# Optimization experiments

Hardware: AMD Instinct MI355X
Metric: run time of the kernel (lower is better)

Reference implementation:

```python
import jax, jax.numpy as jnp
import numpy as np

B, S, D_MODEL, N_HEADS, HEAD_DIM = 4, 2048, 1024, 16, 64
NEG = -1e9


def apply_rope_real(x, cos_f, sin_f):
    # x: [B, H, S, D]; cos_f/sin_f: [S, D//2] broadcast over B, H
    x_even = x[..., ::2]
    x_odd = x[..., 1::2]
    out_even = x_even * cos_f - x_odd * sin_f
    out_odd = x_even * sin_f + x_odd * cos_f
    return jnp.stack([out_even, out_odd], axis=-1).reshape(x.shape)


def setup_inputs() -> dict:
    key = jax.random.key(0)
    ks = jax.random.split(key, 8)
    x = jax.random.normal(ks[0], (B, S, D_MODEL), dtype=jnp.float32)
    # RoPE tables: theta_i = 10000^{-2i/d}, angles = pos * theta
    inv_freq = 1.0 / (10000.0 ** (jnp.arange(0, HEAD_DIM, 2, dtype=jnp.float32) / HEAD_DIM))
    angles = jnp.arange(S, dtype=jnp.float32)[:, None] * inv_freq[None, :]  # [S, D/2]
    cos_freqs = jnp.cos(angles)
    sin_freqs = jnp.sin(angles)
    causal_mask = jnp.where(jnp.tril(jnp.ones((S, S), dtype=bool)), 0.0, NEG).astype(jnp.float32)
    scale = 0.02
    w_q = jax.random.normal(ks[1], (D_MODEL, D_MODEL), dtype=jnp.float32) * scale
    w_k = jax.random.normal(ks[2], (D_MODEL, D_MODEL), dtype=jnp.float32) * scale
    w_v = jax.random.normal(ks[3], (D_MODEL, D_MODEL), dtype=jnp.float32) * scale
    w_o = jax.random.normal(ks[4], (D_MODEL, D_MODEL), dtype=jnp.float32) * scale
    return {"x": x, "cos_freqs": cos_freqs, "sin_freqs": sin_freqs,
            "causal_mask": causal_mask, "w_q": w_q, "w_k": w_k, "w_v": w_v, "w_o": w_o}


def reference(x, cos_freqs, sin_freqs, causal_mask, w_q, w_k, w_v, w_o):
    batch, seq_len, _ = x.shape
    scale = 1.0 / jnp.sqrt(jnp.float32(HEAD_DIM))
    # torch Linear: y = x @ W.T
    def proj(w):
        return (x @ w.T).reshape(batch, seq_len, N_HEADS, HEAD_DIM).transpose(0, 2, 1, 3)
    q = apply_rope_real(proj(w_q), cos_freqs, sin_freqs)
    k = apply_rope_real(proj(w_k), cos_freqs, sin_freqs)
    v = proj(w_v)
    attn = jnp.einsum('bhqd,bhkd->bhqk', q, k) * scale + causal_mask
    attn = jax.nn.softmax(attn, axis=-1)
    out = jnp.einsum('bhqk,bhkd->bhqd', attn, v)
    out = out.transpose(0, 2, 1, 3).reshape(batch, seq_len, -1)
    return out @ w_o.T
```

## Files before the change

### kernel.cpp

```cpp
#include <hip/hip_runtime.h>
#include <stdint.h>

#define B_  4
#define S_  2048
#define DM_ 1024
#define NH_ 16
#define HD_ 64

typedef unsigned short ushort_t;
typedef __bf16 bf16x8 __attribute__((ext_vector_type(8)));
typedef float  floatx4 __attribute__((ext_vector_type(4)));
typedef float  floatx16 __attribute__((ext_vector_type(16)));

__device__ __forceinline__ float bf2f(ushort_t u) {
    union { unsigned int i; float f; } v; v.i = ((unsigned int)u) << 16; return v.f;
}
__device__ __forceinline__ ushort_t f2bf(float f) {
    union { float f; unsigned int i; } v; v.f = f;
    unsigned int x = v.i;
    return (ushort_t)((x + 0x7fffu + ((x >> 16) & 1u)) >> 16);
}
__device__ __forceinline__ unsigned int pack_bf16_trunc(float lo, float hi) {
    union { float f; unsigned int u; } a, b;
    a.f = lo; b.f = hi;
    return __builtin_amdgcn_perm(b.u, a.u, 0x07060302u);
}

__global__ __launch_bounds__(256) void cvt_all_kernel(
    const float* __restrict__ x,  const float* __restrict__ wq,
    const float* __restrict__ wk, const float* __restrict__ wv,
    const float* __restrict__ wo,
    ushort_t* __restrict__ xb,  ushort_t* __restrict__ wqb,
    ushort_t* __restrict__ wkb, ushort_t* __restrict__ wvb,
    ushort_t* __restrict__ wob)
{
    const int blk = blockIdx.x;
    const float* src; ushort_t* dst; int off;
    if (blk < 8192)       { src = x;  dst = xb;  off = blk; }
    else if (blk < 9216)  { src = wq; dst = wqb; off = blk - 8192; }
    else if (blk < 10240) { src = wk; dst = wkb; off = blk - 9216; }
    else if (blk < 11264) { src = wv; dst = wvb; off = blk - 10240; }
    else                  { src = wo; dst = wob; off = blk - 11264; }
    const int i = off * 256 + threadIdx.x;
    float4 v = ((const float4*)src)[i];
    ushort4 o; o.x = f2bf(v.x); o.y = f2bf(v.y); o.z = f2bf(v.z); o.w = f2bf(v.w);
    ((ushort4*)dst)[i] = o;
}

__global__ __launch_bounds__(512, 2) void gemm_bt_kernel(
    const ushort_t* __restrict__ A,
    const ushort_t* __restrict__ B0, const ushort_t* __restrict__ B1,
    const ushort_t* __restrict__ B2,
    void* __restrict__ C0, void* __restrict__ C1, void* __restrict__ C2,
    int M, int N, int K, int mode)
{
    __shared__ ushort_t As[2][16384];
    __shared__ ushort_t Bs[2][16384];

    const int z = blockIdx.z;
    const ushort_t* Bw = z == 0 ? B0 : z == 1 ? B1 : B2;
    void* Cv           = z == 0 ? C0 : z == 1 ? C1 : C2;

    const int tid  = threadIdx.x;
    const int wave = tid >> 6, lane = tid & 63;
    const int l15 = lane & 15, quad = lane >> 4;
    const int wr = wave >> 2, wc = wave & 3;
    const int mbase = blockIdx.x * 256;
    const int nbase = blockIdx.y * 256;
    const int NT = K >> 6;

    const int srow = lane >> 3;
    const int schk = (lane & 7) ^ srow;

    auto stageA = [&](int b, int t, int h) {
#pragma unroll
        for (int j = 0; j < 2; ++j) {
            const int idx = wave * 2 + j;
            const int r = h * 128 + idx * 8 + srow;
            const ushort_t* src = A + (size_t)(mbase + r) * K + t * 64 + schk * 8;
            __builtin_amdgcn_global_load_lds(
                (const __attribute__((address_space(1))) unsigned int*)src,
                (__attribute__((address_space(3))) unsigned int*)(&As[b][h * 8192 + idx * 512 + lane * 8]),
                16, 0, 0);
        }
    };
    auto stageB = [&](int b, int t, int h) {
#pragma unroll
        for (int j = 0; j < 2; ++j) {
            const int idx = wave * 2 + j;
            const int r = h * 128 + idx * 8 + srow;
            const ushort_t* src = Bw + (size_t)(nbase + r) * K + t * 64 + schk * 8;
            __builtin_amdgcn_global_load_lds(
                (const __attribute__((address_space(1))) unsigned int*)src,
                (__attribute__((address_space(3))) unsigned int*)(&Bs[b][h * 8192 + idx * 512 + lane * 8]),
                16, 0, 0);
        }
    };

    floatx4 acc[8][4] = {};

    stageA(0, 0, 0); stageA(0, 0, 1);
    stageB(0, 0, 0); stageB(0, 0, 1);
    stageB(1, 1, 0); stageB(1, 1, 1);
    asm volatile("s_waitcnt vmcnt(4)" ::: "memory");
    __builtin_amdgcn_s_barrier();

    auto do_tile = [&](int t, int bt) {
        bf16x8 a0[2][4], a1[2][4], bv0[2][2], bv1[2][2];
#pragma unroll
        for (int kk = 0; kk < 2; ++kk) {
#pragma unroll
            for (int f = 0; f < 4; ++f) {
                const int row = wr * 128 + f * 16 + l15;
                a0[kk][f] = *(const bf16x8*)&As[bt][row * 64 + (((kk << 2) | quad) ^ (l15 & 7)) * 8];
            }
#pragma unroll
            for (int g = 0; g < 2; ++g) {
                const int row = wc * 64 + g * 16 + l15;
                bv0[kk][g] = *(const bf16x8*)&Bs[bt][row * 64 + (((kk << 2) | quad) ^ (l15 & 7)) * 8];
            }
        }
        if (t + 1 < NT) stageA(bt ^ 1, t + 1, 0);
        __builtin_amdgcn_s_barrier();
        asm volatile("s_waitcnt lgkmcnt(0)" ::: "memory");
        __builtin_amdgcn_s_setprio(1);
#pragma unroll
        for (int kk = 0; kk < 2; ++kk)
#pragma unroll
            for (int mt = 0; mt < 4; ++mt)
#pragma unroll
                for (int nt = 0; nt < 2; ++nt)
                    acc[mt][nt] = __builtin_amdgcn_mfma_f32_16x16x32_bf16(
                        a0[kk][mt], bv0[kk][nt], acc[mt][nt], 0, 0, 0);
        __builtin_amdgcn_s_setprio(0);
        __builtin_amdgcn_s_barrier();

#pragma unroll
        for (int kk = 0; kk < 2; ++kk)
#pragma unroll
            for (int g = 0; g < 2; ++g) {
                const int row = wc * 64 + 32 + g * 16 + l15;
                bv1[kk][g] = *(const bf16x8*)&Bs[bt][row * 64 + (((kk << 2) | quad) ^ (l15 & 7)) * 8];
            }
        if (t + 1 < NT) stageA(bt ^ 1, t + 1, 1);
        __builtin_amdgcn_s_barrier();
        asm volatile("s_waitcnt lgkmcnt(0)" ::: "memory");
        __builtin_amdgcn_s_setprio(1);
#pragma unroll
        for (int kk = 0; kk < 2; ++kk)
#pragma unroll
            for (int mt = 0; mt < 4; ++mt)
#pragma unroll
                for (int nt = 0; nt < 2; ++nt)
                    acc[mt][2 + nt] = __builtin_amdgcn_mfma_f32_16x16x32_bf16(
                        a0[kk][mt], bv1[kk][nt], acc[mt][2 + nt], 0, 0, 0);
        __builtin_amdgcn_s_setprio(0);
        __builtin_amdgcn_s_barrier();

#pragma unroll
        for (int kk = 0; kk < 2; ++kk)
#pragma unroll
            for (int f = 0; f < 4; ++f) {
                const int row = wr * 128 + 64 + f * 16 + l15;
                a1[kk][f] = *(const bf16x8*)&As[bt][row * 64 + (((kk << 2) | quad) ^ (l15 & 7)) * 8];
            }
        if (t + 2 < NT) stageB(bt, t + 2, 0);
        __builtin_amdgcn_s_barrier();
        asm volatile("s_waitcnt lgkmcnt(0)" ::: "memory");
        __builtin_amdgcn_s_setprio(1);
#pragma unroll
        for (int kk = 0; kk < 2; ++kk)
#pragma unroll
            for (int mt = 0; mt < 4; ++mt)
#pragma unroll
                for (int nt = 0; nt < 2; ++nt)
                    acc[4 + mt][2 + nt] = __builtin_amdgcn_mfma_f32_16x16x32_bf16(
                        a1[kk][mt], bv1[kk][nt], acc[4 + mt][2 + nt], 0, 0, 0);
        __builtin_amdgcn_s_setprio(0);
        __builtin_amdgcn_s_barrier();

        if (t + 2 < NT) stageB(bt, t + 2, 1);
        __builtin_amdgcn_s_barrier();
        __builtin_amdgcn_s_setprio(1);
#pragma unroll
        for (int kk = 0; kk < 2; ++kk)
#pragma unroll
            for (int mt = 0; mt < 4; ++mt)
#pragma unroll
                for (int nt = 0; nt < 2; ++nt)
                    acc[4 + mt][nt] = __builtin_amdgcn_mfma_f32_16x16x32_bf16(
                        a1[kk][mt], bv0[kk][nt], acc[4 + mt][nt], 0, 0, 0);
        __builtin_amdgcn_s_setprio(0);
        if (t < NT - 2) { asm volatile("s_waitcnt vmcnt(4)" ::: "memory"); }
        else            { asm volatile("s_waitcnt vmcnt(0)" ::: "memory"); }
        __builtin_amdgcn_s_barrier();
    };

    for (int t = 0; t < NT; t += 2) {
        do_tile(t, 0);
        do_tile(t + 1, 1);
    }

    const bool vtmode = (mode == 0) && (z == 2);
#pragma unroll
    for (int mt = 0; mt < 8; ++mt) {
#pragma unroll
        for (int nt = 0; nt < 4; ++nt) {
            const int col = nbase + wc * 64 + nt * 16 + l15;
            const int m0  = mbase + wr * 128 + mt * 16 + quad * 4;
            if (vtmode) {
                const int b = m0 >> 11, s = m0 & 2047;
                const int hh = col >> 6, d = col & 63;
                uint2 pk;
                pk.x = (unsigned)f2bf(acc[mt][nt][0]) | ((unsigned)f2bf(acc[mt][nt][1]) << 16);
                pk.y = (unsigned)f2bf(acc[mt][nt][2]) | ((unsigned)f2bf(acc[mt][nt][3]) << 16);
                *(uint2*)&((ushort_t*)Cv)[((size_t)((b * NH_ + hh) * HD_ + d)) * S_ + s] = pk;
            } else if (mode == 0) {
#pragma unroll
                for (int r = 0; r < 4; ++r) {
                    const int m = m0 + r;
                    const int b = m >> 11, s = m & 2047;
                    const int hh = col >> 6, d = col & 63;
                    ((ushort_t*)Cv)[(((size_t)(b * NH_ + hh)) * S_ + s) * HD_ + d] =
                        f2bf(acc[mt][nt][r]);
                }
            } else {
#pragma unroll
                for (int r = 0; r < 4; ++r)
                    ((float*)Cv)[(size_t)(m0 + r) * N + col] = acc[mt][nt][r];
            }
        }
    }
}

#define QSCALE 0.1803368801f
__global__ __launch_bounds__(256) void rope_kernel(
    ushort_t* __restrict__ q, ushort_t* __restrict__ k,
    const float* __restrict__ cf, const float* __restrict__ sf)
{
    const int idx = blockIdx.x * 256 + threadIdx.x;
    const int j = idx & 31;
    const int s = (idx >> 5) & (S_ - 1);
    const float c  = cf[s * 32 + j];
    const float sn = sf[s * 32 + j];
    const size_t base = (size_t)idx * 2;
    float qe = bf2f(q[base]), qo = bf2f(q[base + 1]);
    q[base]     = f2bf((qe * c - qo * sn) * QSCALE);
    q[base + 1] = f2bf((qe * sn + qo * c) * QSCALE);
    float ke = bf2f(k[base]), ko = bf2f(k[base + 1]);
    k[base]     = f2bf(ke * c - ko * sn);
    k[base + 1] = f2bf(ke * sn + ko * c);
}

__global__ __launch_bounds__(256, 2) void attn_kernel(
    const ushort_t* __restrict__ Qg, const ushort_t* __restrict__ Kg,
    const ushort_t* __restrict__ Vg, ushort_t* __restrict__ Og)
{
    __shared__ ushort_t Ks[64 * 72];
    __shared__ ushort_t Vt[64 * 72];
    __shared__ ushort_t Pt[4][32 * 64];

    const int pair = blockIdx.x;
    const int bh   = blockIdx.y;
    const int tid  = threadIdx.x;
    const int wave = tid >> 6, lane = tid & 63;
    const int l31 = lane & 31, h = lane >> 5;

    const size_t bh_off = (size_t)bh * S_ * HD_;
    const int trow = tid >> 3;
    const int tcol = (tid & 7) * 8;
    const int pswz = (l31 & 7) << 3;
    const int b_out = bh >> 4, h_out = bh & 15;

#pragma unroll 1
    for (int seg = 0; seg < 2; ++seg) {
        const int qtile = seg ? (15 - pair) : pair;
        const int qbase = qtile * 128;
        const int nkt   = 2 * qtile + 2;
        const int qrow  = qbase + wave * 32 + l31;

        bf16x8 qf[4];
#pragma unroll
        for (int ks = 0; ks < 4; ++ks)
            qf[ks] = *(const bf16x8*)(Qg + bh_off + (size_t)qrow * HD_ + ks * 16 + h * 8);

        float m_run = -1e30f, l_run = 0.f;
        floatx16 o_acc[2] = {};

        for (int kt = 0; kt < nkt; ++kt) {
            const int kbase = kt * 64;
            __syncthreads();
#pragma unroll
            for (int r = 0; r < 2; ++r) {
                const int row = trow + r * 32;
                *(bf16x8*)(Ks + row * 72 + tcol) =
                    *(const bf16x8*)(Kg + bh_off + (size_t)(kbase + row) * HD_ + tcol);
                const int c = tid + r * 256;
                const int d = c >> 3, k0 = (c & 7) * 8;
                bf16x8 vv = *(const bf16x8*)(Vg + bh_off + (size_t)d * S_ + kbase + k0);
                *(bf16x8*)(Vt + d * 72 + (k0 ^ (((d >> 3) & 7) << 3))) = vv;
            }
            __syncthreads();

            if (kbase > qbase + wave * 32 + 31) continue;

            floatx16 st[2] = {};
#pragma unroll
            for (int nt = 0; nt < 2; ++nt) {
                const ushort_t* kr = Ks + (nt * 32 + l31) * 72 + h * 8;
#pragma unroll
                for (int ks = 0; ks < 4; ++ks) {
                    bf16x8 kf = *(const bf16x8*)(kr + ks * 16);
                    st[nt] = __builtin_amdgcn_mfma_f32_32x32x16_bf16(kf, qf[ks], st[nt], 0, 0, 0);
                }
            }
            if (kbase + 63 > qbase + wave * 32) {
#pragma unroll
                for (int nt = 0; nt < 2; ++nt) {
                    const int key0 = kbase + nt * 32 + 4 * h;
#pragma unroll
                    for (int c = 0; c < 4; ++c)
#pragma unroll
                        for (int r = 0; r < 4; ++r)
                            if (key0 + 8 * c + r > qrow) st[nt][c * 4 + r] = -1e9f;
                }
            }
            float mx = st[0][0];
#pragma unroll
            for (int nt = 0; nt < 2; ++nt)
#pragma unroll
                for (int i = 0; i < 16; ++i) mx = fmaxf(mx, st[nt][i]);
            mx = fmaxf(mx, __shfl_xor(mx, 32, 64));
            const float mnew = fmaxf(m_run, mx);
            const float alpha = __builtin_amdgcn_exp2f(m_run - mnew);
            m_run = mnew;
            float sum = 0.f;
#pragma unroll
            for (int nt = 0; nt < 2; ++nt)
#pragma unroll
                for (int i = 0; i < 16; ++i) {
                    const float p = __builtin_amdgcn_exp2f(st[nt][i] - mnew);
                    st[nt][i] = p; sum += p;
                }
            sum += __shfl_xor(sum, 32, 64);
            l_run = l_run * alpha + sum;
#pragma unroll
            for (int dt = 0; dt < 2; ++dt)
#pragma unroll
                for (int i = 0; i < 16; ++i) o_acc[dt][i] *= alpha;

            ushort_t* pr = &Pt[wave][l31 * 64];
#pragma unroll
            for (int nt = 0; nt < 2; ++nt)
#pragma unroll
                for (int c = 0; c < 4; ++c) {
                    uint2 pk;
                    pk.x = pack_bf16_trunc(st[nt][c * 4 + 0], st[nt][c * 4 + 1]);
                    pk.y = pack_bf16_trunc(st[nt][c * 4 + 2], st[nt][c * 4 + 3]);
                    *(uint2*)(pr + (((nt * 32 + 8 * c) ^ pswz) + 4 * h)) = pk;
                }
            __builtin_amdgcn_fence(__ATOMIC_ACQ_REL, "wavefront");
            __builtin_amdgcn_wave_barrier();

            bf16x8 pf[4];
#pragma unroll
            for (int ks = 0; ks < 4; ++ks)
                pf[ks] = *(const bf16x8*)(&Pt[wave][l31 * 64 + ((ks * 16 + h * 8) ^ pswz)]);

#pragma unroll
            for (int dt = 0; dt < 2; ++dt) {
                const int d = dt * 32 + l31;
                const int sw = ((d >> 3) & 7) << 3;
                const ushort_t* vr = Vt + d * 72;
#pragma unroll
                for (int ks = 0; ks < 4; ++ks) {
                    bf16x8 vf = *(const bf16x8*)(vr + ((ks * 16 + h * 8) ^ sw));
                    o_acc[dt] = __builtin_amdgcn_mfma_f32_32x32x16_bf16(vf, pf[ks], o_acc[dt], 0, 0, 0);
                }
            }
        }

        const float inv = 1.0f / l_run;
        ushort_t* orow = Og + ((size_t)(b_out * S_ + qrow)) * DM_ + h_out * HD_;
#pragma unroll
        for (int dt = 0; dt < 2; ++dt)
#pragma unroll
            for (int c = 0; c < 4; ++c) {
                uint2 pk;
                pk.x = (unsigned)f2bf(o_acc[dt][c * 4 + 0] * inv) |
                       ((unsigned)f2bf(o_acc[dt][c * 4 + 1] * inv) << 16);
                pk.y = (unsigned)f2bf(o_acc[dt][c * 4 + 2] * inv) |
                       ((unsigned)f2bf(o_acc[dt][c * 4 + 3] * inv) << 16);
                *(uint2*)(orow + dt * 32 + 8 * c + 4 * h) = pk;
            }
    }
}

extern "C" void kernel_launch(void* const* d_in, const int* in_sizes, int n_in,
                              void* d_out, int out_size, void* d_ws, size_t ws_size,
                              hipStream_t stream)
{
    const float* x  = (const float*)d_in[0];
    const float* cf = (const float*)d_in[1];
    const float* sf = (const float*)d_in[2];
    const float* wq = (const float*)d_in[4];
    const float* wk = (const float*)d_in[5];
    const float* wv = (const float*)d_in[6];
    const float* wo = (const float*)d_in[7];
    float* out = (float*)d_out;

    const size_t NELEM = (size_t)B_ * S_ * DM_;
    const size_t WELEM = (size_t)DM_ * DM_;
    ushort_t* xb  = (ushort_t*)d_ws;
    ushort_t* qb  = xb + NELEM;
    ushort_t* kb  = qb + NELEM;
    ushort_t* vb  = kb + NELEM;
    ushort_t* ao  = vb + NELEM;
    ushort_t* wqb = ao + NELEM;
    ushort_t* wkb = wqb + WELEM;
    ushort_t* wvb = wkb + WELEM;
    ushort_t* wob = wvb + WELEM;

    cvt_all_kernel<<<dim3(8192 + 4 * 1024), 256, 0, stream>>>(
        x, wq, wk, wv, wo, xb, wqb, wkb, wvb, wob);

    const int M = B_ * S_;
    gemm_bt_kernel<<<dim3(M / 256, DM_ / 256, 3), 512, 0, stream>>>(
        xb, wqb, wkb, wvb, qb, kb, vb, M, DM_, DM_, 0);
    rope_kernel<<<dim3((B_ * NH_ * S_ * 32) / 256), 256, 0, stream>>>(qb, kb, cf, sf);
    attn_kernel<<<dim3(8, B_ * NH_), 256, 0, stream>>>(qb, kb, vb, ao);
    gemm_bt_kernel<<<dim3(M / 256, DM_ / 256, 1), 512, 0, stream>>>(
        ao, wob, wob, wob, out, out, out, M, DM_, DM_, 1);
}
```

Measured before the change: 287.3 us.

## Shrink GEMM tile to 256x128 and remap blocks for XCD locality

Changes the projection GEMM tile from 256x256 to 256x128, with an 8-wave 4x2 layout where each wave holds a 64x64 accumulator. Staging loads are reindexed to match. The 3D grid becomes a 1D grid whose block ids are remapped so consecutive work lands on the same XCD (chiplet) for better L2 reuse. The goal is more blocks to fill the CUs and fewer accumulator registers, at the cost of lower arithmetic intensity per block and more reloading of A.

```diff
diff --git a/kernel.cpp b/kernel.cpp
--- a/kernel.cpp
+++ b/kernel.cpp
@@ -52,72 +52,75 @@
     const ushort_t* __restrict__ B0, const ushort_t* __restrict__ B1,
     const ushort_t* __restrict__ B2,
     void* __restrict__ C0, void* __restrict__ C1, void* __restrict__ C2,
-    int M, int N, int K, int mode)
+    int M, int N, int K, int mode, int nz)
 {
     __shared__ ushort_t As[2][16384];
-    __shared__ ushort_t Bs[2][16384];
-
-    const int z = blockIdx.z;
+    __shared__ ushort_t Bs[2][8192];
+
+    const int lid = blockIdx.x;
+    const int cpx = gridDim.x >> 3;
+    const int wg  = (lid & 7) * cpx + (lid >> 3);
+    const int x   = wg / (8 * nz);
+    const int rr  = wg - x * (8 * nz);
+    const int y   = rr & 7;
+    const int z   = rr >> 3;
+
     const ushort_t* Bw = z == 0 ? B0 : z == 1 ? B1 : B2;
     void* Cv           = z == 0 ? C0 : z == 1 ? C1 : C2;
 
     const int tid  = threadIdx.x;
     const int wave = tid >> 6, lane = tid & 63;
     const int l15 = lane & 15, quad = lane >> 4;
-    const int wr = wave >> 2, wc = wave & 3;
-    const int mbase = blockIdx.x * 256;
-    const int nbase = blockIdx.y * 256;
+    const int wr = wave >> 1, wc = wave & 1;
+    const int mbase = x * 256;
+    const int nbase = y * 128;
     const int NT = K >> 6;
 
-    const int srow = lane >> 3;
-    const int schk = (lane & 7) ^ srow;
-
-    auto stageA = [&](int b, int t, int h) {
-#pragma unroll
-        for (int j = 0; j < 2; ++j) {
-            const int idx = wave * 2 + j;
-            const int r = h * 128 + idx * 8 + srow;
-            const ushort_t* src = A + (size_t)(mbase + r) * K + t * 64 + schk * 8;
+    auto stageA = [&](int bt, int t, int L0) {
+#pragma unroll
+        for (int L = L0; L < L0 + 2; ++L) {
+            const int e8  = L * 512 + tid;
+            const int row = e8 >> 3, c = e8 & 7;
+            const ushort_t* src = A + (size_t)(mbase + row) * K + t * 64 + ((c ^ (row & 7)) << 3);
             __builtin_amdgcn_global_load_lds(
                 (const __attribute__((address_space(1))) unsigned int*)src,
-                (__attribute__((address_space(3))) unsigned int*)(&As[b][h * 8192 + idx * 512 + lane * 8]),
-                16, 0, 0);
+                (__attribute__((address_space(3))) unsigned int*)(&As[bt][e8 * 8]), 16, 0, 0);
         }
     };
-    auto stageB = [&](int b, int t, int h) {
-#pragma unroll
-        for (int j = 0; j < 2; ++j) {
-            const int idx = wave * 2 + j;
-            const int r = h * 128 + idx * 8 + srow;
-            const ushort_t* src = Bw + (size_t)(nbase + r) * K + t * 64 + schk * 8;
-            __builtin_amdgcn_global_load_lds(
-                (const __attribute__((address_space(1))) unsigned int*)src,
-                (__attribute__((address_space(3))) unsigned int*)(&Bs[b][h * 8192 + idx * 512 + lane * 8]),
-                16, 0, 0);
-        }
+    auto stageB = [&](int bt, int t, int L) {
+        const int e8  = L * 512 + tid;
+        const int row = e8 >> 3, c = e8 & 7;
+        const ushort_t* src = Bw + (size_t)(nbase + row) * K + t * 64 + ((c ^ (row & 7)) << 3);
+        __builtin_amdgcn_global_load_lds(
+            (const __attribute__((address_space(1))) unsigned int*)src,
+            (__attribute__((address_space(3))) unsigned int*)(&Bs[bt][e8 * 8]), 16, 0, 0);
     };
 
-    floatx4 acc[8][4] = {};
-
-    stageA(0, 0, 0); stageA(0, 0, 1);
+    floatx4 acc[4][4] = {};
+
+    stageA(0, 0, 0); stageA(0, 0, 2);
     stageB(0, 0, 0); stageB(0, 0, 1);
-    stageB(1, 1, 0); stageB(1, 1, 1);
-    asm volatile("s_waitcnt vmcnt(4)" ::: "memory");
+    if (NT > 1) {
+        stageB(1, 1, 0); stageB(1, 1, 1);
+        asm volatile("s_waitcnt vmcnt(2)" ::: "memory");
+    } else {
+        asm volatile("s_waitcnt vmcnt(0)" ::: "memory");
+    }
     __builtin_amdgcn_s_barrier();
 
     auto do_tile = [&](int t, int bt) {
-        bf16x8 a0[2][4], a1[2][4], bv0[2][2], bv1[2][2];
+        bf16x8 a0[2][2], a1[2][2], b0[2][2], b1[2][2];
 #pragma unroll
         for (int kk = 0; kk < 2; ++kk) {
 #pragma unroll
-            for (int f = 0; f < 4; ++f) {
-                const int row = wr * 128 + f * 16 + l15;
-                a0[kk][f] = *(const bf16x8*)&As[bt][row * 64 + (((kk << 2) | quad) ^ (l15 & 7)) * 8];
+            for (int f = 0; f < 2; ++f) {
+                const int row = wr * 64 + f * 16 + l15;
+                a0[kk][f] = *(const bf16x8*)&As[bt][row * 64 + ((((kk << 2) | quad)) ^ (l15 & 7)) * 8];
             }
 #pragma unroll
             for (int g = 0; g < 2; ++g) {
                 const int row = wc * 64 + g * 16 + l15;
-                bv0[kk][g] = *(const bf16x8*)&Bs[bt][row * 64 + (((kk << 2) | quad) ^ (l15 & 7)) * 8];
+                b0[kk][g] = *(const bf16x8*)&Bs[bt][row * 64 + ((((kk << 2) | quad)) ^ (l15 & 7)) * 8];
             }
         }
         if (t + 1 < NT) stageA(bt ^ 1, t + 1, 0);
@@ -127,11 +130,11 @@
 #pragma unroll
         for (int kk = 0; kk < 2; ++kk)
 #pragma unroll
-            for (int mt = 0; mt < 4; ++mt)
+            for (int mt = 0; mt < 2; ++mt)
 #pragma unroll
                 for (int nt = 0; nt < 2; ++nt)
                     acc[mt][nt] = __builtin_amdgcn_mfma_f32_16x16x32_bf16(
-                        a0[kk][mt], bv0[kk][nt], acc[mt][nt], 0, 0, 0);
+                        a0[kk][mt], b0[kk][nt], acc[mt][nt], 0, 0, 0);
         __builtin_amdgcn_s_setprio(0);
         __builtin_amdgcn_s_barrier();
 
@@ -140,29 +143,29 @@
 #pragma unroll
             for (int g = 0; g < 2; ++g) {
                 const int row = wc * 64 + 32 + g * 16 + l15;
-                bv1[kk][g] = *(const bf16x8*)&Bs[bt][row * 64 + (((kk << 2) | quad) ^ (l15 & 7)) * 8];
-            }
-        if (t + 1 < NT) stageA(bt ^ 1, t + 1, 1);
+                b1[kk][g] = *(const bf16x8*)&Bs[bt][row * 64 + ((((kk << 2) | quad)) ^ (l15 & 7)) * 8];
+            }
+        if (t + 1 < NT) stageA(bt ^ 1, t + 1, 2);
         __builtin_amdgcn_s_barrier();
         asm volatile("s_waitcnt lgkmcnt(0)" ::: "memory");
         __builtin_amdgcn_s_setprio(1);
 #pragma unroll
         for (int kk = 0; kk < 2; ++kk)
 #pragma unroll
-            for (int mt = 0; mt < 4; ++mt)
+            for (int mt = 0; mt < 2; ++mt)
 #pragma unroll
                 for (int nt = 0; nt < 2; ++nt)
                     acc[mt][2 + nt] = __builtin_amdgcn_mfma_f32_16x16x32_bf16(
-                        a0[kk][mt], bv1[kk][nt], acc[mt][2 + nt], 0, 0, 0);
+                        a0[kk][mt], b1[kk][nt], acc[mt][2 + nt], 0, 0, 0);
         __builtin_amdgcn_s_setprio(0);
         __builtin_amdgcn_s_barrier();
 
 #pragma unroll
         for (int kk = 0; kk < 2; ++kk)
 #pragma unroll
-            for (int f = 0; f < 4; ++f) {
-                const int row = wr * 128 + 64 + f * 16 + l15;
-                a1[kk][f] = *(const bf16x8*)&As[bt][row * 64 + (((kk << 2) | quad) ^ (l15 & 7)) * 8];
+            for (int f = 0; f < 2; ++f) {
+                const int row = wr * 64 + 32 + f * 16 + l15;
+                a1[kk][f] = *(const bf16x8*)&As[bt][row * 64 + ((((kk << 2) | quad)) ^ (l15 & 7)) * 8];
             }
         if (t + 2 < NT) stageB(bt, t + 2, 0);
         __builtin_amdgcn_s_barrier();
@@ -171,11 +174,11 @@
 #pragma unroll
         for (int kk = 0; kk < 2; ++kk)
 #pragma unroll
-            for (int mt = 0; mt < 4; ++mt)
+            for (int mt = 0; mt < 2; ++mt)
 #pragma unroll
                 for (int nt = 0; nt < 2; ++nt)
-                    acc[4 + mt][2 + nt] = __builtin_amdgcn_mfma_f32_16x16x32_bf16(
-                        a1[kk][mt], bv1[kk][nt], acc[4 + mt][2 + nt], 0, 0, 0);
+                    acc[2 + mt][2 + nt] = __builtin_amdgcn_mfma_f32_16x16x32_bf16(
+                        a1[kk][mt], b1[kk][nt], acc[2 + mt][2 + nt], 0, 0, 0);
         __builtin_amdgcn_s_setprio(0);
         __builtin_amdgcn_s_barrier();
 
@@ -185,13 +188,13 @@
 #pragma unroll
         for (int kk = 0; kk < 2; ++kk)
 #pragma unroll
-            for (int mt = 0; mt < 4; ++mt)
+            for (int mt = 0; mt < 2; ++mt)
 #pragma unroll
                 for (int nt = 0; nt < 2; ++nt)
-                    acc[4 + mt][nt] = __builtin_amdgcn_mfma_f32_16x16x32_bf16(
-                        a1[kk][mt], bv0[kk][nt], acc[4 + mt][nt], 0, 0, 0);
+                    acc[2 + mt][nt] = __builtin_amdgcn_mfma_f32_16x16x32_bf16(
+                        a1[kk][mt], b0[kk][nt], acc[2 + mt][nt], 0, 0, 0);
         __builtin_amdgcn_s_setprio(0);
-        if (t < NT - 2) { asm volatile("s_waitcnt vmcnt(4)" ::: "memory"); }
+        if (t + 2 < NT) { asm volatile("s_waitcnt vmcnt(2)" ::: "memory"); }
         else            { asm volatile("s_waitcnt vmcnt(0)" ::: "memory"); }
         __builtin_amdgcn_s_barrier();
     };
@@ -203,11 +206,11 @@
 
     const bool vtmode = (mode == 0) && (z == 2);
 #pragma unroll
-    for (int mt = 0; mt < 8; ++mt) {
+    for (int mt = 0; mt < 4; ++mt) {
 #pragma unroll
         for (int nt = 0; nt < 4; ++nt) {
             const int col = nbase + wc * 64 + nt * 16 + l15;
-            const int m0  = mbase + wr * 128 + mt * 16 + quad * 4;
+            const int m0  = mbase + wr * 64 + mt * 16 + quad * 4;
             if (vtmode) {
                 const int b = m0 >> 11, s = m0 & 2047;
                 const int hh = col >> 6, d = col & 63;
@@ -425,10 +428,10 @@
         x, wq, wk, wv, wo, xb, wqb, wkb, wvb, wob);
 
     const int M = B_ * S_;
-    gemm_bt_kernel<<<dim3(M / 256, DM_ / 256, 3), 512, 0, stream>>>(
-        xb, wqb, wkb, wvb, qb, kb, vb, M, DM_, DM_, 0);
+    gemm_bt_kernel<<<dim3(32 * 8 * 3), 512, 0, stream>>>(
+        xb, wqb, wkb, wvb, qb, kb, vb, M, DM_, DM_, 0, 3);
     rope_kernel<<<dim3((B_ * NH_ * S_ * 32) / 256), 256, 0, stream>>>(qb, kb, cf, sf);
     attn_kernel<<<dim3(8, B_ * NH_), 256, 0, stream>>>(qb, kb, vb, ao);
-    gemm_bt_kernel<<<dim3(M / 256, DM_ / 256, 1), 512, 0, stream>>>(
-        ao, wob, wob, wob, out, out, out, M, DM_, DM_, 1);
-}
+    gemm_bt_kernel<<<dim3(32 * 8), 512, 0, stream>>>(
+        ao, wob, wob, wob, out, out, out, M, DM_, DM_, 1, 1);
+}
```

New measurement: 282.1 us. About the same (-1.8%).
